# Performance work log

Measured on AMD Instinct MI355X. Metric: run time of the kernel, lower is better.

## Reference

```python
import jax, jax.numpy as jnp
import numpy as np

KSIZE, STRIDES, D_NEURON, DK, DV, NH, DACT, FINAL_DIM = 4, 2, 128, 128, 256, 8, 8, 256
N = KSIZE * KSIZE          # 16 neurons per window
DKH = DK // NH             # 16 == N (required by broadcast in original code)
DVH = DV // NH             # 32


def setup_inputs() -> dict:
    key = jax.random.key(0)
    ks = jax.random.split(key, 12)
    B, H, W, C = 32, 64, 64, 256
    def dense(kw, kb, fan_in, fan_out):
        w = jax.random.normal(kw, (fan_in, fan_out), jnp.float32) / np.sqrt(fan_in)
        b = jnp.zeros((fan_out,), jnp.float32)
        return w, b
    inps = jax.random.normal(ks[0], (B, H, W, C), jnp.float32)
    neuron_emb = jax.random.normal(ks[1], (KSIZE, KSIZE, D_NEURON), jnp.float32) / np.sqrt(D_NEURON)
    wkq_w, wkq_b = dense(ks[2], ks[3], D_NEURON, 2 * DK)
    wv_w, wv_b = dense(ks[4], ks[5], C, DV)
    wgactq_w, wgactq_b = dense(ks[6], ks[7], D_NEURON, DACT)
    wgactk_w, wgactk_b = dense(ks[8], ks[9], C, DACT)
    wf_w, wf_b = dense(ks[10], ks[11], DV, FINAL_DIM)
    return dict(inps=inps, neuron_emb=neuron_emb, wkq_w=wkq_w, wkq_b=wkq_b,
                wv_w=wv_w, wv_b=wv_b, wgactq_w=wgactq_w, wgactq_b=wgactq_b,
                wgactk_w=wgactk_w, wgactk_b=wgactk_b, wf_w=wf_w, wf_b=wf_b)


def _forward(inps, neuron_emb, wkq_w, wkq_b, wv_w, wv_b,
             wgactq_w, wgactq_b, wgactk_w, wgactk_b, wf_w, wf_b):
    B, H, W, C = inps.shape
    # ---- neural structures (tiny, per-head n x n softmax) ----
    kq = neuron_emb @ wkq_w + wkq_b                      # (k,k,2dk)
    k_part, q_part = jnp.split(kq, 2, axis=-1)           # each (k,k,dk)
    flat = lambda t: t.reshape(N, NH, DKH).transpose(1, 0, 2)   # (Nh,n,dkh)
    fk, fq = flat(k_part), flat(q_part)
    # broadcast add requires dkh == n: logits[h,i,j] = fq[h,i,j] + fk[h,j,i]
    logits = fq + fk.transpose(0, 2, 1)                  # (Nh,n,n)
    structures = jax.nn.softmax(logits, axis=-1)
    s0 = structures[:, 0, :]                             # (Nh,n) row 0 per head
    # ---- activation amounts (dacth == 1, i.e. dact == Nh) ----
    actk = inps @ wgactk_w + wgactk_b                    # (B,H,W,Nh)
    actq = (neuron_emb @ wgactq_w + wgactq_b).reshape(N, NH)   # (n,Nh)
    qv = actq[N - 2]                                     # slice [-2:-1] -> (Nh,)
    g = jax.nn.relu(qv[None, None, None, :] + actk)      # (B,H,W,Nh)
    denom = jnp.sum(g, axis=(1, 2), keepdims=True)       # (B,1,1,Nh)
    act = (float(H * W) / (denom + 1e-6)) * g            # (B,H,W,Nh)
    # ---- values, gated per head ----
    v = inps @ wv_w + wv_b                               # (B,H,W,dv)
    v = (v.reshape(B, H, W, NH, DVH) * act[..., None]).reshape(B, H, W, DV)
    # ---- SAME-padded im2col patches (TF extract_patches ordering kh,kw,c) ----
    nH, nW = -(-H // STRIDES), -(-W // STRIDES)
    pad_h = max((nH - 1) * STRIDES + KSIZE - H, 0)
    pad_w = max((nW - 1) * STRIDES + KSIZE - W, 0)
    vp = jnp.pad(v, ((0, 0), (pad_h // 2, pad_h - pad_h // 2),
                     (pad_w // 2, pad_w - pad_w // 2), (0, 0)))
    hi = (nH - 1) * STRIDES + 1
    wi = (nW - 1) * STRIDES + 1
    patches = jnp.stack([vp[:, i:i + hi:STRIDES, j:j + wi:STRIDES, :]
                         for i in range(KSIZE) for j in range(KSIZE)],
                        axis=3)                           # (B,nH,nW,n,dv)
    p = patches.reshape(B, nH, nW, N, NH, DVH)
    # weighted reduce over window positions with structure row 0
    out = jnp.einsum('hn,bxynhd->bxyhd', s0, p).reshape(B, nH, nW, DV)
    return out @ wf_w + wf_b                             # (B,nH,nW,final_dim)


def reference(inps, neuron_emb, wkq_w, wkq_b, wv_w, wv_b,
              wgactq_w, wgactq_b, wgactk_w, wgactk_b, wf_w, wf_b):
    return _forward(inps, neuron_emb, wkq_w, wkq_b, wv_w, wv_b,
                    wgactq_w, wgactq_b, wgactk_w, wgactk_b, wf_w, wf_b)
```

## Files before the change

kernel.cpp:

```cpp
#include <hip/hip_runtime.h>
#include <hip/hip_bf16.h>

#define B_    32
#define H_    64
#define W_    64
#define C_    256
#define NH_   8
#define N_    16
#define PIX_  (B_*H_*W_)
#define OUTPIX_ (B_*32*32)

typedef __hip_bfloat16 bf16;
typedef __attribute__((ext_vector_type(8))) short bf16x8;
typedef __attribute__((ext_vector_type(4))) float f32x4;

__device__ __forceinline__ float bf2f(unsigned short u) {
  union { unsigned int i; float f; } v; v.i = ((unsigned int)u) << 16; return v.f;
}
__device__ __forceinline__ unsigned pk2(float a, float b) {
  union { __hip_bfloat162 h2; unsigned u; } c;
  c.h2 = __float22bfloat162_rn(make_float2(a, b));
  return c.u;
}

__global__ __launch_bounds__(256) void k1_setup(
    const float* __restrict__ emb, const float* __restrict__ wkq_w,
    const float* __restrict__ wkq_b, const float* __restrict__ wgq_w,
    const float* __restrict__ wgq_b,
    float* __restrict__ s0, float* __restrict__ qv) {
  __shared__ float lq[128];
  __shared__ float lk[16][8];
  int t = threadIdx.x;
  if (t < 128) {
    float acc = wkq_b[128 + t];
    for (int e = 0; e < 128; ++e) acc += emb[e] * wkq_w[e * 256 + 128 + t];
    lq[t] = acc;
  } else {
    int idx = t - 128; int j = idx >> 3, h = idx & 7;
    float acc = wkq_b[h * 16];
    for (int e = 0; e < 128; ++e) acc += emb[j * 128 + e] * wkq_w[e * 256 + h * 16];
    lk[j][h] = acc;
  }
  __syncthreads();
  if (t < 8) {
    float l[16]; float m = -1e30f;
    for (int j = 0; j < 16; ++j) { l[j] = lq[t * 16 + j] + lk[j][t]; m = fmaxf(m, l[j]); }
    float s = 0.f;
    for (int j = 0; j < 16; ++j) { l[j] = expf(l[j] - m); s += l[j]; }
    float inv = 1.f / s;
    for (int j = 0; j < 16; ++j) s0[t * 16 + j] = l[j] * inv;
    float acc = wgq_b[t];
    for (int e = 0; e < 128; ++e) acc += emb[14 * 128 + e] * wgq_w[e * 8 + t];
    qv[t] = acc;
  }
}

__global__ __launch_bounds__(256) void prep(
    const float* __restrict__ wv, const float* __restrict__ wf,
    const float* __restrict__ wgk,
    bf16* __restrict__ wvT, bf16* __restrict__ wfT, bf16* __restrict__ wgkT) {
  int bid = blockIdx.x, t = threadIdx.x;
  if (bid < 32) {
    __shared__ unsigned short tile[64][72];
    const float* src = (bid < 16) ? wv : wf;
    bf16* dst = (bid < 16) ? wvT : wfT;
    int tb = bid & 15, tr = tb >> 2, tc = tb & 3;
#pragma unroll
    for (int it = 0; it < 16; ++it) {
      int idx = it * 256 + t, row = idx >> 6, col = idx & 63;
      bf16 h = __float2bfloat16(src[(tr * 64 + row) * 256 + tc * 64 + col]);
      tile[row][col] = *(unsigned short*)&h;
    }
    __syncthreads();
#pragma unroll
    for (int it = 0; it < 16; ++it) {
      int idx = it * 256 + t, row = idx >> 6, col = idx & 63;
      dst[(tc * 64 + row) * 256 + (tr * 64 + col)] = *(bf16*)&tile[col][row];
    }
  } else {
    __shared__ float g[2048];
#pragma unroll
    for (int it = 0; it < 8; ++it) g[it * 256 + t] = wgk[it * 256 + t];
    __syncthreads();
#pragma unroll
    for (int it = 0; it < 16; ++it) {
      int idx = it * 256 + t, a = idx >> 8, k = idx & 255;
      float v = (a < 8) ? g[k * 8 + a] : 0.f;
      wgkT[a * 256 + k] = __float2bfloat16(v);
    }
  }
}

__global__ __launch_bounds__(512) void kA(
    const float* __restrict__ inps, const bf16* __restrict__ wvT,
    const bf16* __restrict__ wgkT, const float* __restrict__ wv_b,
    const float* __restrict__ wgk_b, const float* __restrict__ qv,
    bf16* __restrict__ vraw, float* __restrict__ gbuf,
    float* __restrict__ denom) {
  __shared__ __align__(16) unsigned short ldsA[64][264];
  __shared__ float sden[8];
  __shared__ float qvb_s[8];
  int t = threadIdx.x;
  long pix0 = (long)blockIdx.x * 64;
  if (t < 8) { sden[t] = 0.f; qvb_s[t] = qv[t] + wgk_b[t]; }
  const float* src = inps + pix0 * 256;
#pragma unroll
  for (int it = 0; it < 8; ++it) {
    int idx = it * 512 + t;
    int row = idx >> 6, c4 = (idx & 63) << 2;
    float4 v = *(const float4*)(src + row * 256 + c4);
    *(uint2*)&ldsA[row][c4] = make_uint2(pk2(v.x, v.y), pk2(v.z, v.w));
  }
  __syncthreads();

  int wave = t >> 6, lane = t & 63;
  int mw = wave >> 2, nw = wave & 3;
  int m0 = mw * 32, n0 = nw * 64;
  int lm = lane & 15, q = lane >> 4;
  bool gatew = (nw == 0);

  f32x4 acc[2][4], accg[2];
#pragma unroll
  for (int mf = 0; mf < 2; ++mf) {
    accg[mf] = (f32x4){0.f, 0.f, 0.f, 0.f};
#pragma unroll
    for (int nf = 0; nf < 4; ++nf) acc[mf][nf] = (f32x4){0.f, 0.f, 0.f, 0.f};
  }
  const bf16* brow = wvT + (n0 + lm) * 256;
  const bf16* grow = wgkT + lm * 256;
  const unsigned short* arow0 = &ldsA[m0 + lm][0];
  const unsigned short* arow1 = &ldsA[m0 + 16 + lm][0];

#pragma unroll
  for (int ks = 0; ks < 8; ++ks) {
    int kof = ks * 32 + q * 8;
    bf16x8 a0 = *(const bf16x8*)(arow0 + kof);
    bf16x8 a1 = *(const bf16x8*)(arow1 + kof);
    bf16x8 b0 = *(const bf16x8*)(brow + kof);
    bf16x8 b1 = *(const bf16x8*)(brow + 4096 + kof);
    bf16x8 b2 = *(const bf16x8*)(brow + 8192 + kof);
    bf16x8 b3 = *(const bf16x8*)(brow + 12288 + kof);
    acc[0][0] = __builtin_amdgcn_mfma_f32_16x16x32_bf16(a0, b0, acc[0][0], 0, 0, 0);
    acc[1][0] = __builtin_amdgcn_mfma_f32_16x16x32_bf16(a1, b0, acc[1][0], 0, 0, 0);
    acc[0][1] = __builtin_amdgcn_mfma_f32_16x16x32_bf16(a0, b1, acc[0][1], 0, 0, 0);
    acc[1][1] = __builtin_amdgcn_mfma_f32_16x16x32_bf16(a1, b1, acc[1][1], 0, 0, 0);
    acc[0][2] = __builtin_amdgcn_mfma_f32_16x16x32_bf16(a0, b2, acc[0][2], 0, 0, 0);
    acc[1][2] = __builtin_amdgcn_mfma_f32_16x16x32_bf16(a1, b2, acc[1][2], 0, 0, 0);
    acc[0][3] = __builtin_amdgcn_mfma_f32_16x16x32_bf16(a0, b3, acc[0][3], 0, 0, 0);
    acc[1][3] = __builtin_amdgcn_mfma_f32_16x16x32_bf16(a1, b3, acc[1][3], 0, 0, 0);
    if (gatew) {
      bf16x8 bg = *(const bf16x8*)(grow + kof);
      accg[0] = __builtin_amdgcn_mfma_f32_16x16x32_bf16(a0, bg, accg[0], 0, 0, 0);
      accg[1] = __builtin_amdgcn_mfma_f32_16x16x32_bf16(a1, bg, accg[1], 0, 0, 0);
    }
  }

#pragma unroll
  for (int nf = 0; nf < 4; ++nf) {
    int col = n0 + nf * 16 + lm;
    float wb = wv_b[col];
#pragma unroll
    for (int mf = 0; mf < 2; ++mf) {
#pragma unroll
      for (int r = 0; r < 4; ++r) {
        int rl = m0 + mf * 16 + q * 4 + r;
        vraw[(pix0 + rl) * 256 + col] = __float2bfloat16(acc[mf][nf][r] + wb);
      }
    }
  }

  if (gatew) {
    float part = 0.f;
    if (lm < 8) {
#pragma unroll
      for (int mf = 0; mf < 2; ++mf) {
#pragma unroll
        for (int r = 0; r < 4; ++r) {
          int rl = m0 + mf * 16 + q * 4 + r;
          float gg = fmaxf(qvb_s[lm] + accg[mf][r], 0.f);
          gbuf[(pix0 + rl) * 8 + lm] = gg;
          part += gg;
        }
      }
    }
    part += __shfl_xor(part, 16, 64);
    part += __shfl_xor(part, 32, 64);
    if (lane < 16 && lm < 8) atomicAdd(&sden[lm], part);
  }
  __syncthreads();
  if (t < 8) atomicAdd(&denom[(int)(pix0 >> 12) * 8 + t], sden[t]);
}

__global__ __launch_bounds__(256) void kB(
    const bf16* __restrict__ vraw, const float* __restrict__ s0,
    const float* __restrict__ gbuf, const float* __restrict__ denom,
    const bf16* __restrict__ wfT, const float* __restrict__ wf_b,
    float* __restrict__ out) {
  __shared__ float scfsh[4][64][8];
  __shared__ __align__(16) unsigned short opsh[32][264];
  int t = threadIdx.x;
  int bx = blockIdx.x, b = bx >> 5, x = bx & 31;

  {
    int i = t >> 6, c = t & 63;
    int r = 2 * x + i - 1;
    if (r >= 0 && r < 64) {
      long p = (long)b * 4096 + r * 64 + c;
#pragma unroll
      for (int a = 0; a < 8; ++a)
        scfsh[i][c][a] = 4096.0f / (denom[b * 8 + a] + 1e-6f) * gbuf[p * 8 + a];
    } else {
#pragma unroll
      for (int a = 0; a < 8; ++a) scfsh[i][c][a] = 0.f;
    }
  }
  __syncthreads();

  int c2 = t & 127, yg = t >> 7;
  int h = c2 >> 4;
  float s0r[16];
#pragma unroll
  for (int n = 0; n < 16; ++n) s0r[n] = s0[h * 16 + n];
  const bf16* vsb = vraw + (long)b * (4096 * 256);
  for (int yi = 0; yi < 16; ++yi) {
    int y = yi * 2 + yg;
    float p0 = 0.f, p1 = 0.f;
#pragma unroll
    for (int i = 0; i < 4; ++i) {
      int r = 2 * x + i - 1;
      if (r < 0 || r >= 64) continue;
      const bf16* rowp = vsb + (long)r * 64 * 256 + 2 * c2;
#pragma unroll
      for (int j = 0; j < 4; ++j) {
        int c = 2 * y + j - 1;
        if (c < 0 || c >= 64) continue;
        float coef = s0r[i * 4 + j] * scfsh[i][c][h];
        unsigned u = *(const unsigned*)(rowp + (long)c * 256);
        p0 += coef * bf2f((unsigned short)(u & 0xffff));
        p1 += coef * bf2f((unsigned short)(u >> 16));
      }
    }
    *(unsigned*)&opsh[y][2 * c2] = pk2(p0, p1);
  }
  __syncthreads();

  int wave = t >> 6, lane = t & 63;
  int n0 = wave * 64;
  int lm = lane & 15, q = lane >> 4;
  f32x4 acc[2][4];
#pragma unroll
  for (int mf = 0; mf < 2; ++mf)
#pragma unroll
    for (int nf = 0; nf < 4; ++nf) acc[mf][nf] = (f32x4){0.f, 0.f, 0.f, 0.f};
  const bf16* brow = wfT + (n0 + lm) * 256;
#pragma unroll
  for (int ks = 0; ks < 8; ++ks) {
    int kof = ks * 32 + q * 8;
    bf16x8 a0 = *(const bf16x8*)(&opsh[lm][kof]);
    bf16x8 a1 = *(const bf16x8*)(&opsh[16 + lm][kof]);
#pragma unroll
    for (int nf = 0; nf < 4; ++nf) {
      bf16x8 bb = *(const bf16x8*)(brow + nf * 4096 + kof);
      acc[0][nf] = __builtin_amdgcn_mfma_f32_16x16x32_bf16(a0, bb, acc[0][nf], 0, 0, 0);
      acc[1][nf] = __builtin_amdgcn_mfma_f32_16x16x32_bf16(a1, bb, acc[1][nf], 0, 0, 0);
    }
  }
  long out0 = (long)bx * 32 * 256;
#pragma unroll
  for (int nf = 0; nf < 4; ++nf) {
    int col = n0 + nf * 16 + lm;
    float wb = wf_b[col];
#pragma unroll
    for (int mf = 0; mf < 2; ++mf) {
#pragma unroll
      for (int r = 0; r < 4; ++r) {
        int row = mf * 16 + q * 4 + r;
        out[out0 + row * 256 + col] = acc[mf][nf][r] + wb;
      }
    }
  }
}

extern "C" void kernel_launch(void* const* d_in, const int* in_sizes, int n_in,
                              void* d_out, int out_size, void* d_ws, size_t ws_size,
                              hipStream_t stream) {
  const float* inps  = (const float*)d_in[0];
  const float* emb   = (const float*)d_in[1];
  const float* wkq_w = (const float*)d_in[2];
  const float* wkq_b = (const float*)d_in[3];
  const float* wv_w  = (const float*)d_in[4];
  const float* wv_b  = (const float*)d_in[5];
  const float* wgq_w = (const float*)d_in[6];
  const float* wgq_b = (const float*)d_in[7];
  const float* wgk_w = (const float*)d_in[8];
  const float* wgk_b = (const float*)d_in[9];
  const float* wf_w  = (const float*)d_in[10];
  const float* wf_b  = (const float*)d_in[11];

  float* wsf   = (float*)d_ws;
  float* s0f   = wsf;
  float* qvf   = wsf + 128;
  float* denom = wsf + 256;
  float* gbuf  = wsf + 1024;
  bf16*  wvT   = (bf16*)(wsf + 1049600);
  bf16*  wfT   = (bf16*)(wsf + 1082368);
  bf16*  wgkT  = (bf16*)(wsf + 1115136);
  bf16*  vraw  = (bf16*)(wsf + 1117184);
  float* outp  = (float*)d_out;

  hipMemsetAsync((void*)denom, 0, 1024, stream);
  k1_setup<<<1, 256, 0, stream>>>(emb, wkq_w, wkq_b, wgq_w, wgq_b, s0f, qvf);
  prep<<<33, 256, 0, stream>>>(wv_w, wf_w, wgk_w, wvT, wfT, wgkT);
  kA<<<PIX_ / 64, 512, 0, stream>>>(inps, wvT, wgkT, wv_b, wgk_b, qvf,
                                    vraw, gbuf, denom);
  kB<<<OUTPIX_ / 32, 256, 0, stream>>>(vraw, s0f, gbuf, denom, wfT, wf_b, outp);
}
```

Before: 379.3 us.

## Make kA persistent over four pixel tiles with double-buffered K-half staging

Each kA block now processes four 64-pixel tiles instead of one. The K dimension is split into halves staged through a double-buffered LDS tile, with global loads for the next half issued into registers before the current half's MFMAs. This is meant to overlap the fp32 input fetch with compute and to cut per-block setup and denominator atomics. It adds a barrier per half-tile, and the launch bound requests higher occupancy, which may constrain registers.

```diff
diff --git a/kernel.cpp b/kernel.cpp
--- a/kernel.cpp
+++ b/kernel.cpp
@@ -91,104 +91,139 @@
   }
 }
 
-__global__ __launch_bounds__(512) void kA(
+#define KA_TILES 4
+__global__ __launch_bounds__(512, 4) void kA(
     const float* __restrict__ inps, const bf16* __restrict__ wvT,
     const bf16* __restrict__ wgkT, const float* __restrict__ wv_b,
     const float* __restrict__ wgk_b, const float* __restrict__ qv,
     bf16* __restrict__ vraw, float* __restrict__ gbuf,
     float* __restrict__ denom) {
-  __shared__ __align__(16) unsigned short ldsA[64][264];
+  __shared__ __align__(16) unsigned short ldsA[2][64][136];
   __shared__ float sden[8];
   __shared__ float qvb_s[8];
   int t = threadIdx.x;
-  long pix0 = (long)blockIdx.x * 64;
+  int bid = blockIdx.x;
+  const long px_base = (long)bid * (KA_TILES * 64);
   if (t < 8) { sden[t] = 0.f; qvb_s[t] = qv[t] + wgk_b[t]; }
-  const float* src = inps + pix0 * 256;
-#pragma unroll
-  for (int it = 0; it < 8; ++it) {
-    int idx = it * 512 + t;
-    int row = idx >> 6, c4 = (idx & 63) << 2;
-    float4 v = *(const float4*)(src + row * 256 + c4);
-    *(uint2*)&ldsA[row][c4] = make_uint2(pk2(v.x, v.y), pk2(v.z, v.w));
-  }
-  __syncthreads();
 
   int wave = t >> 6, lane = t & 63;
   int mw = wave >> 2, nw = wave & 3;
   int m0 = mw * 32, n0 = nw * 64;
   int lm = lane & 15, q = lane >> 4;
   bool gatew = (nw == 0);
-
-  f32x4 acc[2][4], accg[2];
-#pragma unroll
-  for (int mf = 0; mf < 2; ++mf) {
-    accg[mf] = (f32x4){0.f, 0.f, 0.f, 0.f};
-#pragma unroll
-    for (int nf = 0; nf < 4; ++nf) acc[mf][nf] = (f32x4){0.f, 0.f, 0.f, 0.f};
-  }
   const bf16* brow = wvT + (n0 + lm) * 256;
   const bf16* grow = wgkT + lm * 256;
-  const unsigned short* arow0 = &ldsA[m0 + lm][0];
-  const unsigned short* arow1 = &ldsA[m0 + 16 + lm][0];
-
-#pragma unroll
-  for (int ks = 0; ks < 8; ++ks) {
-    int kof = ks * 32 + q * 8;
-    bf16x8 a0 = *(const bf16x8*)(arow0 + kof);
-    bf16x8 a1 = *(const bf16x8*)(arow1 + kof);
-    bf16x8 b0 = *(const bf16x8*)(brow + kof);
-    bf16x8 b1 = *(const bf16x8*)(brow + 4096 + kof);
-    bf16x8 b2 = *(const bf16x8*)(brow + 8192 + kof);
-    bf16x8 b3 = *(const bf16x8*)(brow + 12288 + kof);
-    acc[0][0] = __builtin_amdgcn_mfma_f32_16x16x32_bf16(a0, b0, acc[0][0], 0, 0, 0);
-    acc[1][0] = __builtin_amdgcn_mfma_f32_16x16x32_bf16(a1, b0, acc[1][0], 0, 0, 0);
-    acc[0][1] = __builtin_amdgcn_mfma_f32_16x16x32_bf16(a0, b1, acc[0][1], 0, 0, 0);
-    acc[1][1] = __builtin_amdgcn_mfma_f32_16x16x32_bf16(a1, b1, acc[1][1], 0, 0, 0);
-    acc[0][2] = __builtin_amdgcn_mfma_f32_16x16x32_bf16(a0, b2, acc[0][2], 0, 0, 0);
-    acc[1][2] = __builtin_amdgcn_mfma_f32_16x16x32_bf16(a1, b2, acc[1][2], 0, 0, 0);
-    acc[0][3] = __builtin_amdgcn_mfma_f32_16x16x32_bf16(a0, b3, acc[0][3], 0, 0, 0);
-    acc[1][3] = __builtin_amdgcn_mfma_f32_16x16x32_bf16(a1, b3, acc[1][3], 0, 0, 0);
-    if (gatew) {
-      bf16x8 bg = *(const bf16x8*)(grow + kof);
-      accg[0] = __builtin_amdgcn_mfma_f32_16x16x32_bf16(a0, bg, accg[0], 0, 0, 0);
-      accg[1] = __builtin_amdgcn_mfma_f32_16x16x32_bf16(a1, bg, accg[1], 0, 0, 0);
-    }
-  }
-
-#pragma unroll
-  for (int nf = 0; nf < 4; ++nf) {
-    int col = n0 + nf * 16 + lm;
-    float wb = wv_b[col];
-#pragma unroll
-    for (int mf = 0; mf < 2; ++mf) {
-#pragma unroll
-      for (int r = 0; r < 4; ++r) {
-        int rl = m0 + mf * 16 + q * 4 + r;
-        vraw[(pix0 + rl) * 256 + col] = __float2bfloat16(acc[mf][nf][r] + wb);
-      }
-    }
+
+  int sr = t >> 5, sc4 = t & 31;
+  const float* sbase = inps + px_base * 256 + sr * 256 + sc4 * 4;
+  float4 st[4];
+
+#define LOADST(ph_)                                                          \
+  {                                                                          \
+    const float* s_ = sbase + ((ph_) >> 1) * (64 * 256) + ((ph_) & 1) * 128; \
+    _Pragma("unroll")                                                        \
+    for (int it = 0; it < 4; ++it)                                           \
+      st[it] = *(const float4*)(s_ + it * 16 * 256);                         \
+  }
+#define WRITEST(bufi_)                                                       \
+  {                                                                          \
+    _Pragma("unroll")                                                        \
+    for (int it = 0; it < 4; ++it)                                           \
+      *(uint2*)&ldsA[bufi_][it * 16 + sr][sc4 * 4] =                         \
+          make_uint2(pk2(st[it].x, st[it].y), pk2(st[it].z, st[it].w));      \
+  }
+
+  LOADST(0);
+  WRITEST(0);
+  LOADST(1);
+  __syncthreads();
+
+  f32x4 acc[2][4], accg[2];
+  float gsum = 0.f;
+
+#pragma unroll 2
+  for (int ph = 0; ph < 2 * KA_TILES; ++ph) {
+    const int cur = ph & 1;
+    if (cur == 0) {
+#pragma unroll
+      for (int mf = 0; mf < 2; ++mf) {
+        accg[mf] = (f32x4){0.f, 0.f, 0.f, 0.f};
+#pragma unroll
+        for (int nf = 0; nf < 4; ++nf) acc[mf][nf] = (f32x4){0.f, 0.f, 0.f, 0.f};
+      }
+    }
+    const unsigned short* arow0 = &ldsA[cur][m0 + lm][0];
+    const unsigned short* arow1 = &ldsA[cur][m0 + 16 + lm][0];
+#pragma unroll
+    for (int ksl = 0; ksl < 4; ++ksl) {
+      int kof = ksl * 32 + q * 8;
+      bf16x8 a0 = *(const bf16x8*)(arow0 + kof);
+      bf16x8 a1 = *(const bf16x8*)(arow1 + kof);
+      int gk = cur * 128 + kof;
+      bf16x8 b0 = *(const bf16x8*)(brow + gk);
+      bf16x8 b1 = *(const bf16x8*)(brow + 4096 + gk);
+      bf16x8 b2 = *(const bf16x8*)(brow + 8192 + gk);
+      bf16x8 b3 = *(const bf16x8*)(brow + 12288 + gk);
+      acc[0][0] = __builtin_amdgcn_mfma_f32_16x16x32_bf16(a0, b0, acc[0][0], 0, 0, 0);
+      acc[1][0] = __builtin_amdgcn_mfma_f32_16x16x32_bf16(a1, b0, acc[1][0], 0, 0, 0);
+      acc[0][1] = __builtin_amdgcn_mfma_f32_16x16x32_bf16(a0, b1, acc[0][1], 0, 0, 0);
+      acc[1][1] = __builtin_amdgcn_mfma_f32_16x16x32_bf16(a1, b1, acc[1][1], 0, 0, 0);
+      acc[0][2] = __builtin_amdgcn_mfma_f32_16x16x32_bf16(a0, b2, acc[0][2], 0, 0, 0);
+      acc[1][2] = __builtin_amdgcn_mfma_f32_16x16x32_bf16(a1, b2, acc[1][2], 0, 0, 0);
+      acc[0][3] = __builtin_amdgcn_mfma_f32_16x16x32_bf16(a0, b3, acc[0][3], 0, 0, 0);
+      acc[1][3] = __builtin_amdgcn_mfma_f32_16x16x32_bf16(a1, b3, acc[1][3], 0, 0, 0);
+      if (gatew) {
+        bf16x8 bg = *(const bf16x8*)(grow + gk);
+        accg[0] = __builtin_amdgcn_mfma_f32_16x16x32_bf16(a0, bg, accg[0], 0, 0, 0);
+        accg[1] = __builtin_amdgcn_mfma_f32_16x16x32_bf16(a1, bg, accg[1], 0, 0, 0);
+      }
+    }
+
+    if (cur == 1) {
+      long pix0 = px_base + (ph >> 1) * 64;
+#pragma unroll
+      for (int nf = 0; nf < 4; ++nf) {
+        int col = n0 + nf * 16 + lm;
+        float wb = wv_b[col];
+#pragma unroll
+        for (int mf = 0; mf < 2; ++mf) {
+#pragma unroll
+          for (int r = 0; r < 4; ++r) {
+            int rl = m0 + mf * 16 + q * 4 + r;
+            vraw[(pix0 + rl) * 256 + col] = __float2bfloat16(acc[mf][nf][r] + wb);
+          }
+        }
+      }
+      if (gatew && lm < 8) {
+#pragma unroll
+        for (int mf = 0; mf < 2; ++mf) {
+#pragma unroll
+          for (int r = 0; r < 4; ++r) {
+            int rl = m0 + mf * 16 + q * 4 + r;
+            float gg = fmaxf(qvb_s[lm] + accg[mf][r], 0.f);
+            gbuf[(pix0 + rl) * 8 + lm] = gg;
+            gsum += gg;
+          }
+        }
+      }
+    }
+
+    if (ph < 2 * KA_TILES - 1) {
+      WRITEST(cur ^ 1);
+      if (ph < 2 * KA_TILES - 2) LOADST(ph + 2);
+    }
+    __syncthreads();
   }
 
   if (gatew) {
-    float part = 0.f;
-    if (lm < 8) {
-#pragma unroll
-      for (int mf = 0; mf < 2; ++mf) {
-#pragma unroll
-        for (int r = 0; r < 4; ++r) {
-          int rl = m0 + mf * 16 + q * 4 + r;
-          float gg = fmaxf(qvb_s[lm] + accg[mf][r], 0.f);
-          gbuf[(pix0 + rl) * 8 + lm] = gg;
-          part += gg;
-        }
-      }
-    }
-    part += __shfl_xor(part, 16, 64);
-    part += __shfl_xor(part, 32, 64);
-    if (lane < 16 && lm < 8) atomicAdd(&sden[lm], part);
-  }
-  __syncthreads();
-  if (t < 8) atomicAdd(&denom[(int)(pix0 >> 12) * 8 + t], sden[t]);
+    gsum += __shfl_xor(gsum, 16, 64);
+    gsum += __shfl_xor(gsum, 32, 64);
+    if (lane < 8) atomicAdd(&sden[lane], gsum);
+  }
+  __syncthreads();
+  if (t < 8) atomicAdd(&denom[(bid >> 4) * 8 + t], sden[t]);
+#undef LOADST
+#undef WRITEST
 }
 
 __global__ __launch_bounds__(256) void kB(
@@ -311,7 +346,7 @@
   hipMemsetAsync((void*)denom, 0, 1024, stream);
   k1_setup<<<1, 256, 0, stream>>>(emb, wkq_w, wkq_b, wgq_w, wgq_b, s0f, qvf);
   prep<<<33, 256, 0, stream>>>(wv_w, wf_w, wgk_w, wvT, wfT, wgkT);
-  kA<<<PIX_ / 64, 512, 0, stream>>>(inps, wvT, wgkT, wv_b, wgk_b, qvf,
-                                    vraw, gbuf, denom);
+  kA<<<PIX_ / (KA_TILES * 64), 512, 0, stream>>>(inps, wvT, wgkT, wv_b, wgk_b, qvf,
+                                                 vraw, gbuf, denom);
   kB<<<OUTPIX_ / 32, 256, 0, stream>>>(vraw, s0f, gbuf, denom, wfT, wf_b, outp);
 }
```

New measurement: 406.4 us. 1.07x slower.

## Software-pipeline window gather loads and batch GEMM operand loads in kA/kB

Applied to the files above, without the earlier changes.

In kB the window gather now clamps row and column indices and issues all 16 loads for the next output column before computing the current one, using two register buffers. Edge taps are handled by zeroing the coefficient rather than branching. This is meant to hide global-memory latency in the gather. kA splits the LDS A tile into two K-halves, prefetches two K-steps of B and A operands before their MFMAs, and adds a min-blocks launch bound. kB also vectorises the gate load and hoists the denominator reciprocals, at the cost of higher register pressure.

```diff
diff --git a/kernel.cpp b/kernel.cpp
--- a/kernel.cpp
+++ b/kernel.cpp
@@ -91,25 +91,27 @@
   }
 }
 
-__global__ __launch_bounds__(512) void kA(
+__global__ __launch_bounds__(512, 4) void kA(
     const float* __restrict__ inps, const bf16* __restrict__ wvT,
     const bf16* __restrict__ wgkT, const float* __restrict__ wv_b,
     const float* __restrict__ wgk_b, const float* __restrict__ qv,
     bf16* __restrict__ vraw, float* __restrict__ gbuf,
     float* __restrict__ denom) {
-  __shared__ __align__(16) unsigned short ldsA[64][264];
+  __shared__ __align__(16) unsigned short ldsA[2][64][136];
   __shared__ float sden[8];
   __shared__ float qvb_s[8];
   int t = threadIdx.x;
-  long pix0 = (long)blockIdx.x * 64;
+  const long pix0 = (long)blockIdx.x * 64;
   if (t < 8) { sden[t] = 0.f; qvb_s[t] = qv[t] + wgk_b[t]; }
+
   const float* src = inps + pix0 * 256;
 #pragma unroll
   for (int it = 0; it < 8; ++it) {
     int idx = it * 512 + t;
     int row = idx >> 6, c4 = (idx & 63) << 2;
     float4 v = *(const float4*)(src + row * 256 + c4);
-    *(uint2*)&ldsA[row][c4] = make_uint2(pk2(v.x, v.y), pk2(v.z, v.w));
+    *(uint2*)&ldsA[c4 >> 7][row][c4 & 127] =
+        make_uint2(pk2(v.x, v.y), pk2(v.z, v.w));
   }
   __syncthreads();
 
@@ -118,6 +120,8 @@
   int m0 = mw * 32, n0 = nw * 64;
   int lm = lane & 15, q = lane >> 4;
   bool gatew = (nw == 0);
+  const bf16* brow = wvT + (n0 + lm) * 256;
+  const bf16* grow = wgkT + lm * 256;
 
   f32x4 acc[2][4], accg[2];
 #pragma unroll
@@ -126,32 +130,34 @@
 #pragma unroll
     for (int nf = 0; nf < 4; ++nf) acc[mf][nf] = (f32x4){0.f, 0.f, 0.f, 0.f};
   }
-  const bf16* brow = wvT + (n0 + lm) * 256;
-  const bf16* grow = wgkT + lm * 256;
-  const unsigned short* arow0 = &ldsA[m0 + lm][0];
-  const unsigned short* arow1 = &ldsA[m0 + 16 + lm][0];
-
-#pragma unroll
-  for (int ks = 0; ks < 8; ++ks) {
-    int kof = ks * 32 + q * 8;
-    bf16x8 a0 = *(const bf16x8*)(arow0 + kof);
-    bf16x8 a1 = *(const bf16x8*)(arow1 + kof);
-    bf16x8 b0 = *(const bf16x8*)(brow + kof);
-    bf16x8 b1 = *(const bf16x8*)(brow + 4096 + kof);
-    bf16x8 b2 = *(const bf16x8*)(brow + 8192 + kof);
-    bf16x8 b3 = *(const bf16x8*)(brow + 12288 + kof);
-    acc[0][0] = __builtin_amdgcn_mfma_f32_16x16x32_bf16(a0, b0, acc[0][0], 0, 0, 0);
-    acc[1][0] = __builtin_amdgcn_mfma_f32_16x16x32_bf16(a1, b0, acc[1][0], 0, 0, 0);
-    acc[0][1] = __builtin_amdgcn_mfma_f32_16x16x32_bf16(a0, b1, acc[0][1], 0, 0, 0);
-    acc[1][1] = __builtin_amdgcn_mfma_f32_16x16x32_bf16(a1, b1, acc[1][1], 0, 0, 0);
-    acc[0][2] = __builtin_amdgcn_mfma_f32_16x16x32_bf16(a0, b2, acc[0][2], 0, 0, 0);
-    acc[1][2] = __builtin_amdgcn_mfma_f32_16x16x32_bf16(a1, b2, acc[1][2], 0, 0, 0);
-    acc[0][3] = __builtin_amdgcn_mfma_f32_16x16x32_bf16(a0, b3, acc[0][3], 0, 0, 0);
-    acc[1][3] = __builtin_amdgcn_mfma_f32_16x16x32_bf16(a1, b3, acc[1][3], 0, 0, 0);
-    if (gatew) {
-      bf16x8 bg = *(const bf16x8*)(grow + kof);
-      accg[0] = __builtin_amdgcn_mfma_f32_16x16x32_bf16(a0, bg, accg[0], 0, 0, 0);
-      accg[1] = __builtin_amdgcn_mfma_f32_16x16x32_bf16(a1, bg, accg[1], 0, 0, 0);
+
+#pragma unroll
+  for (int sb = 0; sb < 4; ++sb) {
+    bf16x8 A0[2], A1[2], Bv[2][4], Bg[2];
+#pragma unroll
+    for (int k2 = 0; k2 < 2; ++k2) {
+      int ks = sb * 2 + k2;
+      int h = ks >> 2;
+      int kof = (ks & 3) * 32 + q * 8;
+      int gk = ks * 32 + q * 8;
+#pragma unroll
+      for (int nf = 0; nf < 4; ++nf)
+        Bv[k2][nf] = *(const bf16x8*)(brow + nf * 4096 + gk);
+      if (gatew) Bg[k2] = *(const bf16x8*)(grow + gk);
+      A0[k2] = *(const bf16x8*)(&ldsA[h][m0 + lm][kof]);
+      A1[k2] = *(const bf16x8*)(&ldsA[h][m0 + 16 + lm][kof]);
+    }
+#pragma unroll
+    for (int k2 = 0; k2 < 2; ++k2) {
+#pragma unroll
+      for (int nf = 0; nf < 4; ++nf) {
+        acc[0][nf] = __builtin_amdgcn_mfma_f32_16x16x32_bf16(A0[k2], Bv[k2][nf], acc[0][nf], 0, 0, 0);
+        acc[1][nf] = __builtin_amdgcn_mfma_f32_16x16x32_bf16(A1[k2], Bv[k2][nf], acc[1][nf], 0, 0, 0);
+      }
+      if (gatew) {
+        accg[0] = __builtin_amdgcn_mfma_f32_16x16x32_bf16(A0[k2], Bg[k2], accg[0], 0, 0, 0);
+        accg[1] = __builtin_amdgcn_mfma_f32_16x16x32_bf16(A1[k2], Bg[k2], accg[1], 0, 0, 0);
+      }
     }
   }
 
@@ -205,10 +211,20 @@
     int i = t >> 6, c = t & 63;
     int r = 2 * x + i - 1;
     if (r >= 0 && r < 64) {
+      float dn[8];
+#pragma unroll
+      for (int a = 0; a < 8; ++a) dn[a] = 4096.0f / (denom[b * 8 + a] + 1e-6f);
       long p = (long)b * 4096 + r * 64 + c;
-#pragma unroll
-      for (int a = 0; a < 8; ++a)
-        scfsh[i][c][a] = 4096.0f / (denom[b * 8 + a] + 1e-6f) * gbuf[p * 8 + a];
+      const float4* gp = (const float4*)&gbuf[p * 8];
+      float4 g0 = gp[0], g1 = gp[1];
+      scfsh[i][c][0] = dn[0] * g0.x;
+      scfsh[i][c][1] = dn[1] * g0.y;
+      scfsh[i][c][2] = dn[2] * g0.z;
+      scfsh[i][c][3] = dn[3] * g0.w;
+      scfsh[i][c][4] = dn[4] * g1.x;
+      scfsh[i][c][5] = dn[5] * g1.y;
+      scfsh[i][c][6] = dn[6] * g1.z;
+      scfsh[i][c][7] = dn[7] * g1.w;
     } else {
 #pragma unroll
       for (int a = 0; a < 8; ++a) scfsh[i][c][a] = 0.f;
@@ -222,26 +238,59 @@
 #pragma unroll
   for (int n = 0; n < 16; ++n) s0r[n] = s0[h * 16 + n];
   const bf16* vsb = vraw + (long)b * (4096 * 256);
-  for (int yi = 0; yi < 16; ++yi) {
-    int y = yi * 2 + yg;
-    float p0 = 0.f, p1 = 0.f;
-#pragma unroll
-    for (int i = 0; i < 4; ++i) {
-      int r = 2 * x + i - 1;
-      if (r < 0 || r >= 64) continue;
-      const bf16* rowp = vsb + (long)r * 64 * 256 + 2 * c2;
-#pragma unroll
-      for (int j = 0; j < 4; ++j) {
-        int c = 2 * y + j - 1;
-        if (c < 0 || c >= 64) continue;
-        float coef = s0r[i * 4 + j] * scfsh[i][c][h];
-        unsigned u = *(const unsigned*)(rowp + (long)c * 256);
-        p0 += coef * bf2f((unsigned short)(u & 0xffff));
-        p1 += coef * bf2f((unsigned short)(u >> 16));
-      }
-    }
-    *(unsigned*)&opsh[y][2 * c2] = pk2(p0, p1);
-  }
+  const bf16* rp[4];
+#pragma unroll
+  for (int i = 0; i < 4; ++i) {
+    int r = 2 * x + i - 1;
+    int rc = min(max(r, 0), 63);
+    rp[i] = vsb + (long)rc * 64 * 256 + 2 * c2;
+  }
+
+#define LOADYI(U, y_)                                                        \
+  {                                                                          \
+    _Pragma("unroll") for (int i_ = 0; i_ < 4; ++i_) {                       \
+      _Pragma("unroll") for (int j_ = 0; j_ < 4; ++j_) {                     \
+        int c_ = 2 * (y_) + j_ - 1;                                          \
+        int cc_ = min(max(c_, 0), 63);                                       \
+        U[i_][j_] = *(const unsigned*)(rp[i_] + (long)cc_ * 256);            \
+      }                                                                      \
+    }                                                                        \
+  }
+#define COMPYI(U, y_)                                                        \
+  {                                                                          \
+    float p0 = 0.f, p1 = 0.f;                                                \
+    _Pragma("unroll") for (int i_ = 0; i_ < 4; ++i_) {                       \
+      _Pragma("unroll") for (int j_ = 0; j_ < 4; ++j_) {                     \
+        int c_ = 2 * (y_) + j_ - 1;                                          \
+        float coef = (c_ >= 0 && c_ < 64)                                    \
+                         ? s0r[i_ * 4 + j_] * scfsh[i_][c_][h]               \
+                         : 0.f;                                              \
+        unsigned u_ = U[i_][j_];                                             \
+        p0 += coef * bf2f((unsigned short)(u_ & 0xffff));                    \
+        p1 += coef * bf2f((unsigned short)(u_ >> 16));                       \
+      }                                                                      \
+    }                                                                        \
+    *(unsigned*)&opsh[y_][2 * c2] = pk2(p0, p1);                             \
+  }
+
+  {
+    unsigned UA[4][4], UB[4][4];
+    LOADYI(UA, yg);
+#pragma unroll
+    for (int yp = 0; yp < 8; ++yp) {
+      int yA = (2 * yp) * 2 + yg;
+      int yB = (2 * yp + 1) * 2 + yg;
+      LOADYI(UB, yB);
+      COMPYI(UA, yA);
+      if (yp < 7) {
+        int yA2 = (2 * yp + 2) * 2 + yg;
+        LOADYI(UA, yA2);
+      }
+      COMPYI(UB, yB);
+    }
+  }
+#undef LOADYI
+#undef COMPYI
   __syncthreads();
 
   int wave = t >> 6, lane = t & 63;
```

New measurement: 339.5 us. 10.5% less time.
